# Optimization experiments

Hardware: AMD Instinct MI355X
Metric: run time of the kernel (lower is better)

The kernel has to match this reference:

```python
import jax, jax.numpy as jnp
import numpy as np

N_NODES = 100000
N_EDGES = 1600000
N_IN = 256
N_H = 128


def setup_inputs() -> dict:
    key = jax.random.key(0)
    k1, k2, k3, k4 = jax.random.split(key, 4)
    x = jax.random.normal(k1, (N_NODES, N_IN), dtype=jnp.float32)
    edge_index = jax.random.randint(k2, (2, N_EDGES), 0, N_NODES, dtype=jnp.int64)
    # GCNConv weights (glorot-like scale) and biases
    W1 = jax.random.normal(k3, (N_IN, N_H), dtype=jnp.float32) / np.sqrt(N_IN)
    b1 = jnp.zeros((N_H,), dtype=jnp.float32)
    W2 = jax.random.normal(k4, (N_H, N_H), dtype=jnp.float32) / np.sqrt(N_H)
    b2 = jnp.zeros((N_H,), dtype=jnp.float32)
    return {"x": x, "W1": W1, "b1": b1, "W2": W2, "b2": b2, "edge_index": edge_index}


def _gcn_conv(x, W, b, row, col, n_nodes):
    """PyG GCNConv: add self-loops, symmetric norm D^-1/2 A D^-1/2, aggregate at target (col)."""
    h = x @ W  # [N, out]
    # degree including self-loop (edge_weight = 1): deg[i] = 1 + #incoming edges at target i
    deg = jnp.ones((n_nodes,), dtype=x.dtype).at[col].add(1.0)
    dinv = jax.lax.rsqrt(deg)
    # off-diagonal edges: msg j->i weighted by dinv[j]*dinv[i]
    norm = dinv[row] * dinv[col]  # [E]
    msg = h[row] * norm[:, None]  # [E, out]
    agg = jax.ops.segment_sum(msg, col, num_segments=n_nodes)
    # self-loop contribution: weight dinv[i]^2
    agg = agg + h * (dinv * dinv)[:, None]
    return agg + b


def reference(x, W1, b1, W2, b2, edge_index):
    row, col = edge_index[0], edge_index[1]
    n = x.shape[0]
    out = jax.nn.relu(_gcn_conv(x, W1, b1, row, col, n))
    out = _gcn_conv(out, W2, b2, row, col, n)
    return out
```

## Files before the change

kernel.cpp:

```cpp
#include <hip/hip_runtime.h>


#define NN 100000
#define NH 128
#define NB 196
#define SB 256

__device__ __forceinline__ float bf2f(unsigned int u) { return __uint_as_float(u << 16); }
__device__ __forceinline__ unsigned short f2bf(float f) {
    unsigned int u = __float_as_uint(f);
    u = (u + 0x7fffu + ((u >> 16) & 1u)) >> 16;
    return (unsigned short)u;
}

__device__ __forceinline__ void dma16(const void* g, void* l) {
    __builtin_amdgcn_global_load_lds(
        (const __attribute__((address_space(1))) unsigned int*)g,
        (__attribute__((address_space(3))) unsigned int*)l, 16, 0, 0);
}

__global__ __launch_bounds__(256) void k_hist(const int* __restrict__ col,
                                              int* __restrict__ blockCnt, int E, int chb) {
    __shared__ int h[NB];
    int t = threadIdx.x, blk = blockIdx.x;
    if (t < NB) h[t] = 0;
    __syncthreads();
    int s = blk * chb, en = min(E, s + chb);
    for (int e = s + t; e < en; e += 256) atomicAdd(&h[col[e] >> 9], 1);
    __syncthreads();
    if (t < NB) blockCnt[t * SB + blk] = h[t];
}

__global__ __launch_bounds__(256) void k_base(const int* __restrict__ blockCnt,
                                              int* __restrict__ base) {
    __shared__ int s[256];
    int t = threadIdx.x;
    int tot = 0;
    if (t < NB)
        for (int j = 0; j < SB; ++j) tot += blockCnt[t * SB + j];
    s[t] = tot;
    __syncthreads();
    for (int off = 1; off < 256; off <<= 1) {
        int v = (t >= off) ? s[t - off] : 0;
        __syncthreads();
        s[t] += v;
        __syncthreads();
    }
    if (t < NB) base[t] = s[t] - tot;
    if (t == NB - 1) base[NB] = s[t];
}

__global__ __launch_bounds__(256) void k_bscan(const int* __restrict__ blockCnt,
                                               const int* __restrict__ base,
                                               int* __restrict__ blockOff) {
    __shared__ int s[256];
    int t = threadIdx.x, b = blockIdx.x;
    int v = blockCnt[b * SB + t];
    s[t] = v;
    __syncthreads();
    for (int off = 1; off < 256; off <<= 1) {
        int u = (t >= off) ? s[t - off] : 0;
        __syncthreads();
        s[t] += u;
        __syncthreads();
    }
    blockOff[b * SB + t] = base[b] + s[t] - v;
}

__global__ __launch_bounds__(256) void k_scatter(const int* __restrict__ row,
                                                 const int* __restrict__ col,
                                                 const int* __restrict__ blockOff,
                                                 unsigned int* __restrict__ pairs,
                                                 int E, int chb) {
    __shared__ int cur[NB];
    __shared__ int bof[NB];
    int t = threadIdx.x, blk = blockIdx.x;
    if (t < NB) {
        cur[t] = 0;
        bof[t] = blockOff[t * SB + blk];
    }
    __syncthreads();
    int s = blk * chb, en = min(E, s + chb);
    for (int e = s + t; e < en; e += 256) {
        int c = col[e];
        int b = c >> 9;
        int r = atomicAdd(&cur[b], 1);
        pairs[bof[b] + r] = (unsigned int)row[e] | ((unsigned int)(c & 511) << 17);
    }
}

__global__ __launch_bounds__(512) void k_bin(const unsigned int* __restrict__ pairs,
                                             const int* __restrict__ base,
                                             unsigned int* __restrict__ csr,
                                             int* __restrict__ offs,
                                             float* __restrict__ dinv, int n) {
    __shared__ int cnt[512];
    __shared__ int s[512];
    int t = threadIdx.x, b = blockIdx.x;
    cnt[t] = 0;
    __syncthreads();
    int e0 = base[b], e1 = base[b + 1];
    for (int i = e0 + t; i < e1; i += 512) atomicAdd(&cnt[pairs[i] >> 17], 1);
    __syncthreads();
    int v = cnt[t];
    int node = b * 512 + t;
    if (node < n) dinv[node] = rsqrtf(1.0f + (float)v);
    s[t] = v;
    __syncthreads();
    for (int off = 1; off < 512; off <<= 1) {
        int u = (t >= off) ? s[t - off] : 0;
        __syncthreads();
        s[t] += u;
        __syncthreads();
    }
    int excl = s[t] - v;
    if (node <= n) offs[node] = e0 + excl;
    __syncthreads();
    cnt[t] = e0 + excl;
    __syncthreads();
    for (int i = e0 + t; i < e1; i += 512) {
        unsigned int p = pairs[i];
        int d = atomicAdd(&cnt[p >> 17], 1);
        csr[d] = p & 0x1FFFFu;
    }
}

__global__ void k_wprep(const float* __restrict__ W, unsigned short* __restrict__ Thi,
                        unsigned short* __restrict__ Tlo, int K) {
    int idx = blockIdx.x * 256 + threadIdx.x;
    if (idx >= K * 128) return;
    int k = idx >> 7, c = idx & 127;
    float w = W[idx];
    unsigned int u = __float_as_uint(w) & 0xffff0000u;
    float rem = w - __uint_as_float(u);
    Thi[(size_t)c * K + k] = (unsigned short)(u >> 16);
    Tlo[(size_t)c * K + k] = (unsigned short)(__float_as_uint(rem) >> 16);
}

template <int K>
__global__ __launch_bounds__(256) void k_gemm_mfma(const float* __restrict__ A,
                                                   const unsigned short* __restrict__ Bhi,
                                                   const unsigned short* __restrict__ Blo,
                                                   const float* __restrict__ dinv,
                                                   unsigned short* __restrict__ C, int M) {
    using bf16x8 = __attribute__((ext_vector_type(8))) short;
    using f32x4  = __attribute__((ext_vector_type(4))) float;
    constexpr int T = K / 32;
    __shared__ uint4 sA4[2][1024];
    __shared__ uint4 sB4[2][2][512];

    const int lane = threadIdx.x & 63;
    const int wv   = threadIdx.x >> 6;
    const int r    = lane & 15;
    const int kb   = lane >> 4;
    const int rowBase = blockIdx.x * 128;

    f32x4 acc[2][8];
#pragma unroll
    for (int m = 0; m < 2; ++m)
#pragma unroll
        for (int t = 0; t < 8; ++t) acc[m][t] = (f32x4){0.f, 0.f, 0.f, 0.f};

#pragma unroll
    for (int ks = 0; ks < T; ++ks) {
        const int buf = ks & 1;
        const int kk  = ks * 32;
#pragma unroll
        for (int c = 0; c < 4; ++c) {
            int sb = wv * 256 + c * 64;
            int s  = sb + lane;
            int akb = s >> 8, aj = (s >> 7) & 1, ar = s & 127;
            int gr = rowBase + ar; if (gr >= M) gr = M - 1;
            dma16(A + (size_t)gr * K + kk + akb * 8 + aj * 4, &sA4[buf][sb]);
        }
#pragma unroll
        for (int hl = 0; hl < 2; ++hl) {
            const unsigned short* Bp = hl ? Blo : Bhi;
#pragma unroll
            for (int c = 0; c < 2; ++c) {
                int sb = wv * 128 + c * 64;
                int s  = sb + lane;
                int bkb = s >> 7, bcol = s & 127;
                dma16(Bp + (size_t)bcol * K + kk + bkb * 8, &sB4[buf][hl][sb]);
            }
        }
        __syncthreads();
        bf16x8 ah[2], al[2];
#pragma unroll
        for (int m = 0; m < 2; ++m) {
            int rowl = wv * 32 + m * 16 + r;
            uint4 u0 = sA4[buf][kb * 256 + rowl];
            uint4 u1 = sA4[buf][kb * 256 + 128 + rowl];
            float f[8];
            *(uint4*)&f[0] = u0;
            *(uint4*)&f[4] = u1;
#pragma unroll
            for (int j = 0; j < 8; ++j) {
                float x = f[j];
                unsigned int u = __float_as_uint(x) & 0xffff0000u;
                ah[m][j] = (short)(u >> 16);
                al[m][j] = (short)(__float_as_uint(x - __uint_as_float(u)) >> 16);
            }
        }
#pragma unroll
        for (int t = 0; t < 8; ++t) {
            int col = t * 16 + r;
            bf16x8 bh = *(const bf16x8*)&sB4[buf][0][kb * 128 + col];
            bf16x8 bl = *(const bf16x8*)&sB4[buf][1][kb * 128 + col];
#pragma unroll
            for (int m = 0; m < 2; ++m) {
                acc[m][t] = __builtin_amdgcn_mfma_f32_16x16x32_bf16(ah[m], bh, acc[m][t], 0, 0, 0);
                acc[m][t] = __builtin_amdgcn_mfma_f32_16x16x32_bf16(al[m], bh, acc[m][t], 0, 0, 0);
                acc[m][t] = __builtin_amdgcn_mfma_f32_16x16x32_bf16(ah[m], bl, acc[m][t], 0, 0, 0);
            }
        }
    }
    const int wrow = rowBase + wv * 32;
#pragma unroll
    for (int m = 0; m < 2; ++m) {
#pragma unroll
        for (int q = 0; q < 4; ++q) {
            int orow = wrow + m * 16 + kb * 4 + q;
            if (orow < M) {
                float dv = dinv[orow];
#pragma unroll
                for (int t = 0; t < 8; ++t)
                    C[(size_t)orow * 128 + t * 16 + r] = f2bf(acc[m][t][q] * dv);
            }
        }
    }
}

template <int K>
__global__ __launch_bounds__(256) void k_gemm_bf16(const unsigned short* __restrict__ A,
                                                   const unsigned short* __restrict__ Bhi,
                                                   const unsigned short* __restrict__ Blo,
                                                   const float* __restrict__ dinv,
                                                   unsigned short* __restrict__ C, int M) {
    using bf16x8 = __attribute__((ext_vector_type(8))) short;
    using f32x4  = __attribute__((ext_vector_type(4))) float;
    constexpr int T = K / 32;
    __shared__ uint4 sA2[2][512];
    __shared__ uint4 sB4[2][2][512];

    const int lane = threadIdx.x & 63;
    const int wv   = threadIdx.x >> 6;
    const int r    = lane & 15;
    const int kb   = lane >> 4;
    const int rowBase = blockIdx.x * 128;

    f32x4 acc[2][8];
#pragma unroll
    for (int m = 0; m < 2; ++m)
#pragma unroll
        for (int t = 0; t < 8; ++t) acc[m][t] = (f32x4){0.f, 0.f, 0.f, 0.f};

#pragma unroll
    for (int ks = 0; ks < T; ++ks) {
        const int buf = ks & 1;
        const int kk  = ks * 32;
#pragma unroll
        for (int c = 0; c < 2; ++c) {
            int sb = wv * 128 + c * 64;
            int s  = sb + lane;
            int akb = s >> 7, ar = s & 127;
            int gr = rowBase + ar; if (gr >= M) gr = M - 1;
            dma16(A + (size_t)gr * K + kk + akb * 8, &sA2[buf][sb]);
        }
#pragma unroll
        for (int hl = 0; hl < 2; ++hl) {
            const unsigned short* Bp = hl ? Blo : Bhi;
#pragma unroll
            for (int c = 0; c < 2; ++c) {
                int sb = wv * 128 + c * 64;
                int s  = sb + lane;
                int bkb = s >> 7, bcol = s & 127;
                dma16(Bp + (size_t)bcol * K + kk + bkb * 8, &sB4[buf][hl][sb]);
            }
        }
        __syncthreads();
#pragma unroll
        for (int t = 0; t < 8; ++t) {
            int col = t * 16 + r;
            bf16x8 bh = *(const bf16x8*)&sB4[buf][0][kb * 128 + col];
            bf16x8 bl = *(const bf16x8*)&sB4[buf][1][kb * 128 + col];
#pragma unroll
            for (int m = 0; m < 2; ++m) {
                bf16x8 a = *(const bf16x8*)&sA2[buf][kb * 128 + wv * 32 + m * 16 + r];
                acc[m][t] = __builtin_amdgcn_mfma_f32_16x16x32_bf16(a, bh, acc[m][t], 0, 0, 0);
                acc[m][t] = __builtin_amdgcn_mfma_f32_16x16x32_bf16(a, bl, acc[m][t], 0, 0, 0);
            }
        }
    }
    const int wrow = rowBase + wv * 32;
#pragma unroll
    for (int m = 0; m < 2; ++m) {
#pragma unroll
        for (int q = 0; q < 4; ++q) {
            int orow = wrow + m * 16 + kb * 4 + q;
            if (orow < M) {
                float dv = dinv[orow];
#pragma unroll
                for (int t = 0; t < 8; ++t)
                    C[(size_t)orow * 128 + t * 16 + r] = f2bf(acc[m][t][q] * dv);
            }
        }
    }
}

template <bool RELU, bool BF16OUT>
__global__ __launch_bounds__(256) void k_agg(const unsigned short* __restrict__ hb,
                                             const float* __restrict__ dinv,
                                             const int* __restrict__ off,
                                             const unsigned int* __restrict__ csr,
                                             const float* __restrict__ bias,
                                             void* __restrict__ outv, int n) {
    int gid  = blockIdx.x * 256 + threadIdx.x;
    int node = gid >> 4;
    int lane = gid & 15;
    if (node >= n) return;
    float di = dinv[node];
    uint4 us = *(const uint4*)(hb + ((size_t)node << 7) + lane * 8);
    float a[8];
    a[0] = bf2f(us.x & 0xffffu); a[1] = bf2f(us.x >> 16);
    a[2] = bf2f(us.y & 0xffffu); a[3] = bf2f(us.y >> 16);
    a[4] = bf2f(us.z & 0xffffu); a[5] = bf2f(us.z >> 16);
    a[6] = bf2f(us.w & 0xffffu); a[7] = bf2f(us.w >> 16);
    int e  = off[node];
    int e1 = off[node + 1];
    for (; e + 4 <= e1; e += 4) {
        unsigned int s0 = csr[e + 0];
        unsigned int s1 = csr[e + 1];
        unsigned int s2 = csr[e + 2];
        unsigned int s3 = csr[e + 3];
        uint4 u0 = *(const uint4*)(hb + ((size_t)s0 << 7) + lane * 8);
        uint4 u1 = *(const uint4*)(hb + ((size_t)s1 << 7) + lane * 8);
        uint4 u2 = *(const uint4*)(hb + ((size_t)s2 << 7) + lane * 8);
        uint4 u3 = *(const uint4*)(hb + ((size_t)s3 << 7) + lane * 8);
        a[0] += bf2f(u0.x & 0xffffu); a[1] += bf2f(u0.x >> 16);
        a[2] += bf2f(u0.y & 0xffffu); a[3] += bf2f(u0.y >> 16);
        a[4] += bf2f(u0.z & 0xffffu); a[5] += bf2f(u0.z >> 16);
        a[6] += bf2f(u0.w & 0xffffu); a[7] += bf2f(u0.w >> 16);
        a[0] += bf2f(u1.x & 0xffffu); a[1] += bf2f(u1.x >> 16);
        a[2] += bf2f(u1.y & 0xffffu); a[3] += bf2f(u1.y >> 16);
        a[4] += bf2f(u1.z & 0xffffu); a[5] += bf2f(u1.z >> 16);
        a[6] += bf2f(u1.w & 0xffffu); a[7] += bf2f(u1.w >> 16);
        a[0] += bf2f(u2.x & 0xffffu); a[1] += bf2f(u2.x >> 16);
        a[2] += bf2f(u2.y & 0xffffu); a[3] += bf2f(u2.y >> 16);
        a[4] += bf2f(u2.z & 0xffffu); a[5] += bf2f(u2.z >> 16);
        a[6] += bf2f(u2.w & 0xffffu); a[7] += bf2f(u2.w >> 16);
        a[0] += bf2f(u3.x & 0xffffu); a[1] += bf2f(u3.x >> 16);
        a[2] += bf2f(u3.y & 0xffffu); a[3] += bf2f(u3.y >> 16);
        a[4] += bf2f(u3.z & 0xffffu); a[5] += bf2f(u3.z >> 16);
        a[6] += bf2f(u3.w & 0xffffu); a[7] += bf2f(u3.w >> 16);
    }
    for (; e < e1; ++e) {
        unsigned int s = csr[e];
        uint4 u = *(const uint4*)(hb + ((size_t)s << 7) + lane * 8);
        a[0] += bf2f(u.x & 0xffffu); a[1] += bf2f(u.x >> 16);
        a[2] += bf2f(u.y & 0xffffu); a[3] += bf2f(u.y >> 16);
        a[4] += bf2f(u.z & 0xffffu); a[5] += bf2f(u.z >> 16);
        a[6] += bf2f(u.w & 0xffffu); a[7] += bf2f(u.w >> 16);
    }
    float4 b0 = *(const float4*)&bias[lane * 8];
    float4 b1 = *(const float4*)&bias[lane * 8 + 4];
    a[0] = a[0] * di + b0.x; a[1] = a[1] * di + b0.y;
    a[2] = a[2] * di + b0.z; a[3] = a[3] * di + b0.w;
    a[4] = a[4] * di + b1.x; a[5] = a[5] * di + b1.y;
    a[6] = a[6] * di + b1.z; a[7] = a[7] * di + b1.w;
    if (RELU) {
#pragma unroll
        for (int j = 0; j < 8; ++j) a[j] = fmaxf(a[j], 0.f);
    }
    if (BF16OUT) {
        uint4 o;
        o.x = (unsigned int)f2bf(a[0]) | ((unsigned int)f2bf(a[1]) << 16);
        o.y = (unsigned int)f2bf(a[2]) | ((unsigned int)f2bf(a[3]) << 16);
        o.z = (unsigned int)f2bf(a[4]) | ((unsigned int)f2bf(a[5]) << 16);
        o.w = (unsigned int)f2bf(a[6]) | ((unsigned int)f2bf(a[7]) << 16);
        *(uint4*)((unsigned short*)outv + ((size_t)node << 7) + lane * 8) = o;
    } else {
        float* op = (float*)outv + ((size_t)node << 7) + lane * 8;
        *(float4*)op       = make_float4(a[0], a[1], a[2], a[3]);
        *(float4*)(op + 4) = make_float4(a[4], a[5], a[6], a[7]);
    }
}

extern "C" void kernel_launch(void* const* d_in, const int* in_sizes, int n_in,
                              void* d_out, int out_size, void* d_ws, size_t ws_size,
                              hipStream_t stream) {
    const float* x  = (const float*)d_in[0];
    const float* W1 = (const float*)d_in[1];
    const float* b1 = (const float*)d_in[2];
    const float* W2 = (const float*)d_in[3];
    const float* b2 = (const float*)d_in[4];
    const int*   ei = (const int*)d_in[5];

    const int n = NN;
    const int E = in_sizes[5] / 2;
    const int* row = ei;
    const int* col = ei + E;

    char* ws = (char*)d_ws;
    size_t o = 0;
    auto alloc = [&](size_t bytes) {
        void* p = ws + o;
        o = (o + bytes + 255) & ~(size_t)255;
        return p;
    };
    int*            blockCnt = (int*)alloc((size_t)NB * SB * 4);
    int*            blockOff = (int*)alloc((size_t)NB * SB * 4);
    int*            base     = (int*)alloc((size_t)(NB + 1) * 4);
    int*            offs     = (int*)alloc((size_t)(n + 1) * 4);
    float*          dinv     = (float*)alloc((size_t)n * 4);
    unsigned int*   pairs    = (unsigned int*)alloc((size_t)E * 4);
    unsigned int*   csr      = (unsigned int*)alloc((size_t)E * 4);
    unsigned short* bufH     = (unsigned short*)alloc((size_t)n * NH * 2);
    unsigned short* bufG     = (unsigned short*)alloc((size_t)n * NH * 2);
    unsigned short* wt1hi    = (unsigned short*)alloc(256 * 128 * 2);
    unsigned short* wt1lo    = (unsigned short*)alloc(256 * 128 * 2);
    unsigned short* wt2hi    = (unsigned short*)alloc(128 * 128 * 2);
    unsigned short* wt2lo    = (unsigned short*)alloc(128 * 128 * 2);

    const int chb = (E + SB - 1) / SB;

    k_wprep<<<(256 * 128 + 255) / 256, 256, 0, stream>>>(W1, wt1hi, wt1lo, 256);
    k_wprep<<<(128 * 128 + 255) / 256, 256, 0, stream>>>(W2, wt2hi, wt2lo, 128);

    k_hist<<<SB, 256, 0, stream>>>(col, blockCnt, E, chb);
    k_base<<<1, 256, 0, stream>>>(blockCnt, base);
    k_bscan<<<NB, 256, 0, stream>>>(blockCnt, base, blockOff);
    k_scatter<<<SB, 256, 0, stream>>>(row, col, blockOff, pairs, E, chb);
    k_bin<<<NB, 512, 0, stream>>>(pairs, base, csr, offs, dinv, n);

    int aggBlocks = (n + 15) / 16;
    int gemmBlocks = (n + 127) / 128;
    k_gemm_mfma<256><<<gemmBlocks, 256, 0, stream>>>(x, wt1hi, wt1lo, dinv, bufH, n);
    k_agg<true, true><<<aggBlocks, 256, 0, stream>>>(bufH, dinv, offs, csr, b1, bufG, n);
    k_gemm_bf16<128><<<gemmBlocks, 256, 0, stream>>>(bufG, wt2hi, wt2lo, dinv, bufH, n);
    k_agg<false, false><<<aggBlocks, 256, 0, stream>>>(bufH, dinv, offs, csr, b2, d_out, n);
}
```

Measured before the change: 254.8 us.

## Prefetch next GEMM K-tile during MFMA and unroll aggregation gather by eight

Both MFMA GEMM kernels now issue the async global-to-LDS loads for the next K tile before computing on the current double buffer, with a barrier at the end of each step. This is meant to overlap load latency with MFMA work, which the old load-then-sync-then-compute order could not do. Separately, the aggregation kernel gathers eight neighbour rows per iteration instead of four to put more memory requests in flight, at the cost of more registers.

```diff
diff --git a/kernel.cpp b/kernel.cpp
--- a/kernel.cpp
+++ b/kernel.cpp
@@ -155,23 +155,15 @@
     const int kb   = lane >> 4;
     const int rowBase = blockIdx.x * 128;
 
-    f32x4 acc[2][8];
-#pragma unroll
-    for (int m = 0; m < 2; ++m)
-#pragma unroll
-        for (int t = 0; t < 8; ++t) acc[m][t] = (f32x4){0.f, 0.f, 0.f, 0.f};
-
-#pragma unroll
-    for (int ks = 0; ks < T; ++ks) {
-        const int buf = ks & 1;
-        const int kk  = ks * 32;
+    auto stage = [&](int ks, int b) {
+        const int kk = ks * 32;
 #pragma unroll
         for (int c = 0; c < 4; ++c) {
             int sb = wv * 256 + c * 64;
             int s  = sb + lane;
             int akb = s >> 8, aj = (s >> 7) & 1, ar = s & 127;
             int gr = rowBase + ar; if (gr >= M) gr = M - 1;
-            dma16(A + (size_t)gr * K + kk + akb * 8 + aj * 4, &sA4[buf][sb]);
+            dma16(A + (size_t)gr * K + kk + akb * 8 + aj * 4, &sA4[b][sb]);
         }
 #pragma unroll
         for (int hl = 0; hl < 2; ++hl) {
@@ -181,10 +173,23 @@
                 int sb = wv * 128 + c * 64;
                 int s  = sb + lane;
                 int bkb = s >> 7, bcol = s & 127;
-                dma16(Bp + (size_t)bcol * K + kk + bkb * 8, &sB4[buf][hl][sb]);
-            }
-        }
-        __syncthreads();
+                dma16(Bp + (size_t)bcol * K + kk + bkb * 8, &sB4[b][hl][sb]);
+            }
+        }
+    };
+
+    f32x4 acc[2][8];
+#pragma unroll
+    for (int m = 0; m < 2; ++m)
+#pragma unroll
+        for (int t = 0; t < 8; ++t) acc[m][t] = (f32x4){0.f, 0.f, 0.f, 0.f};
+
+    stage(0, 0);
+    __syncthreads();
+#pragma unroll
+    for (int ks = 0; ks < T; ++ks) {
+        const int buf = ks & 1;
+        if (ks + 1 < T) stage(ks + 1, buf ^ 1);
         bf16x8 ah[2], al[2];
 #pragma unroll
         for (int m = 0; m < 2; ++m) {
@@ -214,6 +219,7 @@
                 acc[m][t] = __builtin_amdgcn_mfma_f32_16x16x32_bf16(ah[m], bl, acc[m][t], 0, 0, 0);
             }
         }
+        __syncthreads();
     }
     const int wrow = rowBase + wv * 32;
 #pragma unroll
@@ -249,23 +255,15 @@
     const int kb   = lane >> 4;
     const int rowBase = blockIdx.x * 128;
 
-    f32x4 acc[2][8];
-#pragma unroll
-    for (int m = 0; m < 2; ++m)
-#pragma unroll
-        for (int t = 0; t < 8; ++t) acc[m][t] = (f32x4){0.f, 0.f, 0.f, 0.f};
-
-#pragma unroll
-    for (int ks = 0; ks < T; ++ks) {
-        const int buf = ks & 1;
-        const int kk  = ks * 32;
+    auto stage = [&](int ks, int b) {
+        const int kk = ks * 32;
 #pragma unroll
         for (int c = 0; c < 2; ++c) {
             int sb = wv * 128 + c * 64;
             int s  = sb + lane;
             int akb = s >> 7, ar = s & 127;
             int gr = rowBase + ar; if (gr >= M) gr = M - 1;
-            dma16(A + (size_t)gr * K + kk + akb * 8, &sA2[buf][sb]);
+            dma16(A + (size_t)gr * K + kk + akb * 8, &sA2[b][sb]);
         }
 #pragma unroll
         for (int hl = 0; hl < 2; ++hl) {
@@ -275,10 +273,23 @@
                 int sb = wv * 128 + c * 64;
                 int s  = sb + lane;
                 int bkb = s >> 7, bcol = s & 127;
-                dma16(Bp + (size_t)bcol * K + kk + bkb * 8, &sB4[buf][hl][sb]);
-            }
-        }
-        __syncthreads();
+                dma16(Bp + (size_t)bcol * K + kk + bkb * 8, &sB4[b][hl][sb]);
+            }
+        }
+    };
+
+    f32x4 acc[2][8];
+#pragma unroll
+    for (int m = 0; m < 2; ++m)
+#pragma unroll
+        for (int t = 0; t < 8; ++t) acc[m][t] = (f32x4){0.f, 0.f, 0.f, 0.f};
+
+    stage(0, 0);
+    __syncthreads();
+#pragma unroll
+    for (int ks = 0; ks < T; ++ks) {
+        const int buf = ks & 1;
+        if (ks + 1 < T) stage(ks + 1, buf ^ 1);
 #pragma unroll
         for (int t = 0; t < 8; ++t) {
             int col = t * 16 + r;
@@ -291,6 +302,7 @@
                 acc[m][t] = __builtin_amdgcn_mfma_f32_16x16x32_bf16(a, bl, acc[m][t], 0, 0, 0);
             }
         }
+        __syncthreads();
     }
     const int wrow = rowBase + wv * 32;
 #pragma unroll
@@ -307,6 +319,12 @@
         }
     }
 }
+
+#define ACC8(u)                                              \
+    a[0] += bf2f(u.x & 0xffffu); a[1] += bf2f(u.x >> 16);    \
+    a[2] += bf2f(u.y & 0xffffu); a[3] += bf2f(u.y >> 16);    \
+    a[4] += bf2f(u.z & 0xffffu); a[5] += bf2f(u.z >> 16);    \
+    a[6] += bf2f(u.w & 0xffffu); a[7] += bf2f(u.w >> 16);
 
 template <bool RELU, bool BF16OUT>
 __global__ __launch_bounds__(256) void k_agg(const unsigned short* __restrict__ hb,
@@ -328,39 +346,31 @@
     a[6] = bf2f(us.w & 0xffffu); a[7] = bf2f(us.w >> 16);
     int e  = off[node];
     int e1 = off[node + 1];
-    for (; e + 4 <= e1; e += 4) {
-        unsigned int s0 = csr[e + 0];
-        unsigned int s1 = csr[e + 1];
-        unsigned int s2 = csr[e + 2];
-        unsigned int s3 = csr[e + 3];
+    for (; e + 8 <= e1; e += 8) {
+        unsigned int s0 = csr[e + 0], s1 = csr[e + 1], s2 = csr[e + 2], s3 = csr[e + 3];
+        unsigned int s4 = csr[e + 4], s5 = csr[e + 5], s6 = csr[e + 6], s7 = csr[e + 7];
         uint4 u0 = *(const uint4*)(hb + ((size_t)s0 << 7) + lane * 8);
         uint4 u1 = *(const uint4*)(hb + ((size_t)s1 << 7) + lane * 8);
         uint4 u2 = *(const uint4*)(hb + ((size_t)s2 << 7) + lane * 8);
         uint4 u3 = *(const uint4*)(hb + ((size_t)s3 << 7) + lane * 8);
-        a[0] += bf2f(u0.x & 0xffffu); a[1] += bf2f(u0.x >> 16);
-        a[2] += bf2f(u0.y & 0xffffu); a[3] += bf2f(u0.y >> 16);
-        a[4] += bf2f(u0.z & 0xffffu); a[5] += bf2f(u0.z >> 16);
-        a[6] += bf2f(u0.w & 0xffffu); a[7] += bf2f(u0.w >> 16);
-        a[0] += bf2f(u1.x & 0xffffu); a[1] += bf2f(u1.x >> 16);
-        a[2] += bf2f(u1.y & 0xffffu); a[3] += bf2f(u1.y >> 16);
-        a[4] += bf2f(u1.z & 0xffffu); a[5] += bf2f(u1.z >> 16);
-        a[6] += bf2f(u1.w & 0xffffu); a[7] += bf2f(u1.w >> 16);
-        a[0] += bf2f(u2.x & 0xffffu); a[1] += bf2f(u2.x >> 16);
-        a[2] += bf2f(u2.y & 0xffffu); a[3] += bf2f(u2.y >> 16);
-        a[4] += bf2f(u2.z & 0xffffu); a[5] += bf2f(u2.z >> 16);
-        a[6] += bf2f(u2.w & 0xffffu); a[7] += bf2f(u2.w >> 16);
-        a[0] += bf2f(u3.x & 0xffffu); a[1] += bf2f(u3.x >> 16);
-        a[2] += bf2f(u3.y & 0xffffu); a[3] += bf2f(u3.y >> 16);
-        a[4] += bf2f(u3.z & 0xffffu); a[5] += bf2f(u3.z >> 16);
-        a[6] += bf2f(u3.w & 0xffffu); a[7] += bf2f(u3.w >> 16);
+        uint4 u4 = *(const uint4*)(hb + ((size_t)s4 << 7) + lane * 8);
+        uint4 u5 = *(const uint4*)(hb + ((size_t)s5 << 7) + lane * 8);
+        uint4 u6 = *(const uint4*)(hb + ((size_t)s6 << 7) + lane * 8);
+        uint4 u7 = *(const uint4*)(hb + ((size_t)s7 << 7) + lane * 8);
+        ACC8(u0) ACC8(u1) ACC8(u2) ACC8(u3) ACC8(u4) ACC8(u5) ACC8(u6) ACC8(u7)
+    }
+    for (; e + 4 <= e1; e += 4) {
+        unsigned int s0 = csr[e + 0], s1 = csr[e + 1], s2 = csr[e + 2], s3 = csr[e + 3];
+        uint4 u0 = *(const uint4*)(hb + ((size_t)s0 << 7) + lane * 8);
+        uint4 u1 = *(const uint4*)(hb + ((size_t)s1 << 7) + lane * 8);
+        uint4 u2 = *(const uint4*)(hb + ((size_t)s2 << 7) + lane * 8);
+        uint4 u3 = *(const uint4*)(hb + ((size_t)s3 << 7) + lane * 8);
+        ACC8(u0) ACC8(u1) ACC8(u2) ACC8(u3)
     }
     for (; e < e1; ++e) {
         unsigned int s = csr[e];
         uint4 u = *(const uint4*)(hb + ((size_t)s << 7) + lane * 8);
-        a[0] += bf2f(u.x & 0xffffu); a[1] += bf2f(u.x >> 16);
-        a[2] += bf2f(u.y & 0xffffu); a[3] += bf2f(u.y >> 16);
-        a[4] += bf2f(u.z & 0xffffu); a[5] += bf2f(u.z >> 16);
-        a[6] += bf2f(u.w & 0xffffu); a[7] += bf2f(u.w >> 16);
+        ACC8(u)
     }
     float4 b0 = *(const float4*)&bias[lane * 8];
     float4 b1 = *(const float4*)&bias[lane * 8 + 4];
```

After: 255.0 us. About the same (+0.1%).
